# Optimization experiments

Measured on AMD Instinct MI355X. Metric: run time of the kernel, lower is better.

Reference implementation:

```python
import jax, jax.numpy as jnp
import numpy as np

C, H, W = 8, 8, 8
A = 6            # action_dim
LATENT = 64
HID = 64
GRU_IN = HID + A + LATENT  # 134


def _conv(x, w):
    return jax.lax.conv_general_dilated(
        x, w, (1, 1), 'VALID', dimension_numbers=('NCHW', 'OIHW', 'NCHW'))


def setup_inputs() -> dict:
    key = jax.random.key(0)
    ks = jax.random.split(key, 20)
    B, N, T = 64, 10, 128
    s_h = jax.random.normal(ks[0], (B, N, T, C, H, W), jnp.float32)
    a_h = jax.random.randint(ks[1], (B, N, T), 0, A).astype(jnp.int64)
    b_z = jax.random.normal(ks[2], (B, LATENT), jnp.float32)
    s = 0.05
    p = {
        'conv1_w': jax.random.normal(ks[3], (32, C, 3, 3)) * s,
        'conv1_b': jnp.zeros((32,)),
        'conv2_w': jax.random.normal(ks[4], (32, 32, 3, 3)) * s,
        'conv2_b': jnp.zeros((32,)),
        'fc_w': jax.random.normal(ks[5], (HID, 32 * 4 * 4)) * s,
        'fc_b': jnp.zeros((HID,)),
        'emb': jax.random.normal(ks[6], (A, A)) * s,
        'gru_wih': jax.random.normal(ks[7], (3 * HID, GRU_IN)) * s,
        'gru_whh': jax.random.normal(ks[8], (3 * HID, HID)) * s,
        'gru_bih': jnp.zeros((3 * HID,)),
        'gru_bhh': jnp.zeros((3 * HID,)),
        'mlp1_w': jax.random.normal(ks[9], (HID, HID)) * s,
        'mlp1_b': jnp.zeros((HID,)),
        'mlp2_w': jax.random.normal(ks[10], (A, HID)) * s,
        'mlp2_b': jnp.zeros((A,)),
    }
    return {'s_h': s_h, 'a_h': a_h, 'b_z': b_z, **p}


def reference(s_h, a_h, b_z, conv1_w, conv1_b, conv2_w, conv2_b, fc_w, fc_b,
              emb, gru_wih, gru_whh, gru_bih, gru_bhh,
              mlp1_w, mlp1_b, mlp2_w, mlp2_b):
    B, N = s_h.shape[0], s_h.shape[1]
    T = a_h.shape[2]
    BN = B * N

    # action mask, [B, N, T, 1]
    action_masks = (a_h != A - 1)[..., None].astype(jnp.float32)

    # --- state encoder on first frame only ---
    s0 = s_h[:, :, 0].reshape(BN, C, H, W)
    x = jax.nn.relu(_conv(s0, conv1_w) + conv1_b[:, None, None])
    x = jax.nn.relu(_conv(x, conv2_w) + conv2_b[:, None, None])
    x = x.reshape(BN, -1)                       # [BN, 512]
    state_emb = jax.nn.relu(x @ fc_w.T + fc_b)  # [BN, HID]

    bz = jnp.broadcast_to(b_z[:, None, :], (B, N, LATENT)).reshape(BN, LATENT)

    h0 = jnp.zeros((BN, HID), s_h.dtype)
    act0 = jnp.full((BN,), A - 1, jnp.int32)

    def step(carry, _):
        h, act = carry
        a_emb = emb[act]                                          # [BN, A]
        inp = jnp.concatenate([state_emb, a_emb, bz], axis=-1)    # [BN, GRU_IN]
        gx = inp @ gru_wih.T + gru_bih
        gh = h @ gru_whh.T + gru_bhh
        xr, xz, xn = jnp.split(gx, 3, axis=-1)
        hr, hz, hn = jnp.split(gh, 3, axis=-1)
        r = jax.nn.sigmoid(xr + hr)
        z = jax.nn.sigmoid(xz + hz)
        n = jnp.tanh(xn + r * hn)
        h_new = (1.0 - z) * n + z * h
        hid = jnp.tanh(h_new @ mlp1_w.T + mlp1_b)
        logits = hid @ mlp2_w.T + mlp2_b                          # [BN, A]
        next_act = jax.lax.stop_gradient(jnp.argmax(logits, axis=-1)).astype(jnp.int32)
        return (h_new, next_act), logits

    (_, _), logits_seq = jax.lax.scan(step, (h0, act0), None, length=T - 1)
    # logits_seq: [T-1, BN, A] -> [B, N, T-1, A]
    logits_all = jnp.transpose(logits_seq, (1, 0, 2)).reshape(B, N, T - 1, A)
    return logits_all, action_masks
```

## Files before the change

kernel.cpp:

```cpp
#include <hip/hip_runtime.h>

#define A_DIM 6
#define HID_D 64
#define LATENT_D 64
#define GRU_IN_D 134
#define T_STEPS 128
#define N_ENV 10
#define BN_TOT 640

typedef float f2 __attribute__((ext_vector_type(2)));

__device__ __forceinline__ float fast_sigmoid(float x) {
    return __builtin_amdgcn_rcpf(1.0f + __builtin_amdgcn_exp2f(-1.4426950408889634f * x));
}
__device__ __forceinline__ float fast_tanh(float x) {
    return 1.0f - 2.0f * __builtin_amdgcn_rcpf(1.0f + __builtin_amdgcn_exp2f(2.8853900817779268f * x));
}

template<int CTRL>
__device__ __forceinline__ float dppadd(float v) {
    int t = __builtin_amdgcn_update_dpp(0, __builtin_bit_cast(int, v), CTRL, 0xf, 0xf, true);
    return v + __builtin_bit_cast(float, t);
}
__device__ __forceinline__ float wave_reduce_add(float v) {
    v = dppadd<0x111>(v);
    v = dppadd<0x112>(v);
    v = dppadd<0x114>(v);
    v = dppadd<0x118>(v);
    v = dppadd<0x142>(v);
    v = dppadd<0x143>(v);
    return __builtin_bit_cast(float, __builtin_amdgcn_readlane(__builtin_bit_cast(int, v), 63));
}

__global__ __launch_bounds__(128, 1)
void policy_kernel(const float* __restrict__ s_h,
                   const int*   __restrict__ a_h,
                   const float* __restrict__ b_z,
                   const float* __restrict__ conv1_w, const float* __restrict__ conv1_b,
                   const float* __restrict__ conv2_w, const float* __restrict__ conv2_b,
                   const float* __restrict__ fc_w,    const float* __restrict__ fc_b,
                   const float* __restrict__ emb,
                   const float* __restrict__ gru_wih, const float* __restrict__ gru_whh,
                   const float* __restrict__ gru_bih, const float* __restrict__ gru_bhh,
                   const float* __restrict__ mlp1_w,  const float* __restrict__ mlp1_b,
                   const float* __restrict__ mlp2_w,  const float* __restrict__ mlp2_b,
                   float* __restrict__ logits_out, float* __restrict__ mask_out)
{
    __shared__ __align__(16) float s0[512];
    __shared__ __align__(16) float a1[1152];
    __shared__ __align__(16) float a2[512];
    __shared__ __align__(16) float pfc[128];
    __shared__ __align__(16) float semb[64];
    __shared__ __align__(16) float gxc[192];
    __shared__ __align__(16) float atab[6*192];
    __shared__ __align__(16) float hspec[6*64];

    const int bn  = blockIdx.x;
    const int tid = threadIdx.x;
    const int j   = tid & 63;
    const int w   = tid >> 6;

    mask_out[bn * T_STEPS + tid] = (a_h[bn * T_STEPS + tid] != (A_DIM - 1)) ? 1.0f : 0.0f;

    {
        const float* src = s_h + (size_t)bn * T_STEPS * 512;
        #pragma unroll
        for (int i = 0; i < 4; ++i) s0[tid + i * 128] = src[tid + i * 128];
    }
    __syncthreads();

    for (int i = tid; i < 1152; i += 128) {
        const int oc = i / 36, r = i % 36, oh = r / 6, ow = r % 6;
        float sum = conv1_b[oc];
        const float* wp = conv1_w + oc * 72;
        #pragma unroll
        for (int ic = 0; ic < 8; ++ic)
            #pragma unroll
            for (int kh = 0; kh < 3; ++kh)
                #pragma unroll
                for (int kw = 0; kw < 3; ++kw)
                    sum = fmaf(s0[ic * 64 + (oh + kh) * 8 + (ow + kw)],
                               wp[ic * 9 + kh * 3 + kw], sum);
        a1[i] = fmaxf(sum, 0.0f);
    }
    __syncthreads();

    for (int i = tid; i < 512; i += 128) {
        const int oc = i / 16, r = i % 16, oh = r / 4, ow = r % 4;
        float sum = conv2_b[oc];
        const float* wp = conv2_w + oc * 288;
        for (int ic = 0; ic < 32; ++ic)
            #pragma unroll
            for (int kh = 0; kh < 3; ++kh)
                #pragma unroll
                for (int kw = 0; kw < 3; ++kw)
                    sum = fmaf(a1[ic * 36 + (oh + kh) * 6 + (ow + kw)],
                               wp[ic * 9 + kh * 3 + kw], sum);
        a2[i] = fmaxf(sum, 0.0f);
    }
    __syncthreads();

    {
        const float* wp = fc_w + j * 512 + w * 256;
        const float* ap = a2 + w * 256;
        float s0a = 0.f, s1a = 0.f, s2a = 0.f, s3a = 0.f;
        for (int k = 0; k < 256; k += 4) {
            s0a = fmaf(ap[k + 0], wp[k + 0], s0a);
            s1a = fmaf(ap[k + 1], wp[k + 1], s1a);
            s2a = fmaf(ap[k + 2], wp[k + 2], s2a);
            s3a = fmaf(ap[k + 3], wp[k + 3], s3a);
        }
        pfc[tid] = (s0a + s1a) + (s2a + s3a);
    }
    __syncthreads();
    if (tid < 64) semb[tid] = fmaxf(pfc[tid] + pfc[tid + 64] + fc_b[tid], 0.0f);
    __syncthreads();

    {
        const float* bz = b_z + (size_t)(bn / N_ENV) * LATENT_D;
        for (int g = tid; g < 192; g += 128) {
            float sum = gru_bih[g] + ((g < 128) ? gru_bhh[g] : 0.0f);
            const float* wp = gru_wih + g * GRU_IN_D;
            for (int k = 0; k < 64; ++k) sum = fmaf(semb[k], wp[k], sum);
            for (int k = 0; k < 64; ++k) sum = fmaf(bz[k], wp[70 + k], sum);
            gxc[g] = sum;
        }
    }
    for (int i = tid; i < 6 * 192; i += 128) {
        const int a = i / 192, g = i % 192;
        float sum = 0.0f;
        #pragma unroll
        for (int q = 0; q < 6; ++q)
            sum = fmaf(emb[a * 6 + q], gru_wih[g * GRU_IN_D + 64 + q], sum);
        atab[i] = sum;
    }
    __syncthreads();

    if (w == 1) return;

    f2 wr[32], wz[32], wn[32], w1[32];
    {
        const float* pr = gru_whh + (size_t)j * 64;
        const float* pz = gru_whh + (size_t)(64 + j) * 64;
        const float* pn = gru_whh + (size_t)(128 + j) * 64;
        const float* p1 = mlp1_w + (size_t)j * 64;
        #pragma unroll
        for (int i = 0; i < 16; ++i) {
            float4 v;
            v = ((const float4*)pr)[i]; wr[2*i] = (f2){v.x, v.y}; wr[2*i+1] = (f2){v.z, v.w};
            v = ((const float4*)pz)[i]; wz[2*i] = (f2){v.x, v.y}; wz[2*i+1] = (f2){v.z, v.w};
            v = ((const float4*)pn)[i]; wn[2*i] = (f2){v.x, v.y}; wn[2*i+1] = (f2){v.z, v.w};
            v = ((const float4*)p1)[i]; w1[2*i] = (f2){v.x, v.y}; w1[2*i+1] = (f2){v.z, v.w};
        }
    }
    const float bhn = gru_bhh[128 + j];
    const float b1j = mlp1_b[j];
    float arx[6], azx[6], anx[6], m2c[6], b2[6];
    {
        const float gxr = gxc[j], gxz = gxc[64 + j], gxn = gxc[128 + j];
        #pragma unroll
        for (int a = 0; a < 6; ++a) {
            arx[a] = gxr + atab[a * 192 + j];
            azx[a] = gxz + atab[a * 192 + 64 + j];
            anx[a] = gxn + atab[a * 192 + 128 + j];
            m2c[a] = mlp2_w[a * 64 + j];
            b2[a] = mlp2_b[a];
        }
    }

    float ha[6];
    #pragma unroll
    for (int a = 0; a < 6; ++a) {
        const float r = fast_sigmoid(arx[a]);
        const float z = fast_sigmoid(azx[a]);
        const float n = fast_tanh(fmaf(r, bhn, anx[a]));
        ha[a] = fmaf(z, 0.0f - n, n);
    }
    __builtin_amdgcn_wave_barrier();
    #pragma unroll
    for (int a = 0; a < 6; ++a) hspec[a * 64 + j] = ha[a];
    __builtin_amdgcn_wave_barrier();

    int act = A_DIM - 1;
    float* lout = logits_out + (size_t)bn * (T_STEPS - 1) * A_DIM;

    for (int t = 0; t < T_STEPS - 1; ++t) {
        const float4* hb = (const float4*)(hspec + (act << 6));
        float hprev = ha[0];
        #pragma unroll
        for (int a = 1; a < 6; ++a) hprev = (act == a) ? ha[a] : hprev;

        f2 p1a = {0.f, 0.f}, p1b = {0.f, 0.f};
        f2 pr = {0.f, 0.f}, pz = {0.f, 0.f}, pn = {0.f, 0.f};
        #pragma unroll
        for (int i = 0; i < 16; ++i) {
            const float4 hv = hb[i];
            const f2 haa = (f2){hv.x, hv.y};
            const f2 hcc = (f2){hv.z, hv.w};
            p1a += haa * w1[2*i]; p1b += hcc * w1[2*i+1];
            pr += haa * wr[2*i]; pr += hcc * wr[2*i+1];
            pz += haa * wz[2*i]; pz += hcc * wz[2*i+1];
            pn += haa * wn[2*i]; pn += hcc * wn[2*i+1];
        }
        const f2 p1 = p1a + p1b;
        const float hid = fast_tanh(p1.x + p1.y + b1j);
        const float hr = pr.x + pr.y;
        const float hz = pz.x + pz.y;
        const float hn = pn.x + pn.y + bhn;

        const float l0 = wave_reduce_add(hid * m2c[0]) + b2[0];
        const float l1 = wave_reduce_add(hid * m2c[1]) + b2[1];
        const float l2 = wave_reduce_add(hid * m2c[2]) + b2[2];
        const float l3 = wave_reduce_add(hid * m2c[3]) + b2[3];
        const float l4 = wave_reduce_add(hid * m2c[4]) + b2[4];
        const float l5 = wave_reduce_add(hid * m2c[5]) + b2[5];

        #pragma unroll
        for (int a = 0; a < 6; ++a) {
            const float r = fast_sigmoid(arx[a] + hr);
            const float z = fast_sigmoid(azx[a] + hz);
            const float n = fast_tanh(fmaf(r, hn, anx[a]));
            ha[a] = fmaf(z, hprev - n, n);
        }
        __builtin_amdgcn_wave_barrier();
        #pragma unroll
        for (int a = 0; a < 6; ++a) hspec[a * 64 + j] = ha[a];
        __builtin_amdgcn_wave_barrier();

        float best = l0; int bi = 0;
        if (l1 > best) { best = l1; bi = 1; }
        if (l2 > best) { best = l2; bi = 2; }
        if (l3 > best) { best = l3; bi = 3; }
        if (l4 > best) { best = l4; bi = 4; }
        if (l5 > best) { best = l5; bi = 5; }
        act = bi;

        if (j < A_DIM) {
            const float outv = (j == 0) ? l0 : (j == 1) ? l1 : (j == 2) ? l2
                             : (j == 3) ? l3 : (j == 4) ? l4 : l5;
            lout[t * A_DIM + j] = outv;
        }
    }
}

extern "C" void kernel_launch(void* const* d_in, const int* in_sizes, int n_in,
                              void* d_out, int out_size, void* d_ws, size_t ws_size,
                              hipStream_t stream) {
    const float* s_h     = (const float*)d_in[0];
    const int*   a_h     = (const int*)  d_in[1];
    const float* b_z     = (const float*)d_in[2];
    const float* conv1_w = (const float*)d_in[3];
    const float* conv1_b = (const float*)d_in[4];
    const float* conv2_w = (const float*)d_in[5];
    const float* conv2_b = (const float*)d_in[6];
    const float* fc_w    = (const float*)d_in[7];
    const float* fc_b    = (const float*)d_in[8];
    const float* emb     = (const float*)d_in[9];
    const float* gru_wih = (const float*)d_in[10];
    const float* gru_whh = (const float*)d_in[11];
    const float* gru_bih = (const float*)d_in[12];
    const float* gru_bhh = (const float*)d_in[13];
    const float* mlp1_w  = (const float*)d_in[14];
    const float* mlp1_b  = (const float*)d_in[15];
    const float* mlp2_w  = (const float*)d_in[16];
    const float* mlp2_b  = (const float*)d_in[17];

    float* out = (float*)d_out;
    float* logits_out = out;
    float* mask_out   = out + (size_t)BN_TOT * (T_STEPS - 1) * A_DIM;

    policy_kernel<<<BN_TOT, 128, 0, stream>>>(
        s_h, a_h, b_z, conv1_w, conv1_b, conv2_w, conv2_b, fc_w, fc_b, emb,
        gru_wih, gru_whh, gru_bih, gru_bhh, mlp1_w, mlp1_b, mlp2_w, mlp2_b,
        logits_out, mask_out);
}
```

Measured before the change: 484.0 us.

## Shrink blocks to one wave and compute action-embedding projections in registers

Cuts each block from two waves to one 64-thread wave. The encoder prologue (conv1, conv2, fc) now runs serially on that single wave, and the split-K fc reduction through shared memory is gone. The shared atab table is replaced by per-lane register computation of the action-embedding contributions, which removes a shared buffer and a barrier. This frees CU resources that the idle second wave used to hold during the recurrent loop, at the cost of a longer prologue per block.

```diff
diff --git a/kernel.cpp b/kernel.cpp
--- a/kernel.cpp
+++ b/kernel.cpp
@@ -32,7 +32,7 @@
     return __builtin_bit_cast(float, __builtin_amdgcn_readlane(__builtin_bit_cast(int, v), 63));
 }
 
-__global__ __launch_bounds__(128, 1)
+__global__ __launch_bounds__(64) __attribute__((amdgpu_waves_per_eu(1, 1)))
 void policy_kernel(const float* __restrict__ s_h,
                    const int*   __restrict__ a_h,
                    const float* __restrict__ b_z,
@@ -49,27 +49,28 @@
     __shared__ __align__(16) float s0[512];
     __shared__ __align__(16) float a1[1152];
     __shared__ __align__(16) float a2[512];
-    __shared__ __align__(16) float pfc[128];
     __shared__ __align__(16) float semb[64];
     __shared__ __align__(16) float gxc[192];
-    __shared__ __align__(16) float atab[6*192];
     __shared__ __align__(16) float hspec[6*64];
 
     const int bn  = blockIdx.x;
     const int tid = threadIdx.x;
-    const int j   = tid & 63;
-    const int w   = tid >> 6;
-
-    mask_out[bn * T_STEPS + tid] = (a_h[bn * T_STEPS + tid] != (A_DIM - 1)) ? 1.0f : 0.0f;
+    const int j   = tid;
+
+    #pragma unroll
+    for (int i = 0; i < 2; ++i) {
+        const int t = tid + i * 64;
+        mask_out[bn * T_STEPS + t] = (a_h[bn * T_STEPS + t] != (A_DIM - 1)) ? 1.0f : 0.0f;
+    }
 
     {
         const float* src = s_h + (size_t)bn * T_STEPS * 512;
         #pragma unroll
-        for (int i = 0; i < 4; ++i) s0[tid + i * 128] = src[tid + i * 128];
-    }
-    __syncthreads();
-
-    for (int i = tid; i < 1152; i += 128) {
+        for (int i = 0; i < 8; ++i) s0[tid + i * 64] = src[tid + i * 64];
+    }
+    __syncthreads();
+
+    for (int i = tid; i < 1152; i += 64) {
         const int oc = i / 36, r = i % 36, oh = r / 6, ow = r % 6;
         float sum = conv1_b[oc];
         const float* wp = conv1_w + oc * 72;
@@ -85,7 +86,7 @@
     }
     __syncthreads();
 
-    for (int i = tid; i < 512; i += 128) {
+    for (int i = tid; i < 512; i += 64) {
         const int oc = i / 16, r = i % 16, oh = r / 4, ow = r % 4;
         float sum = conv2_b[oc];
         const float* wp = conv2_w + oc * 288;
@@ -101,24 +102,21 @@
     __syncthreads();
 
     {
-        const float* wp = fc_w + j * 512 + w * 256;
-        const float* ap = a2 + w * 256;
+        const float* wp = fc_w + j * 512;
         float s0a = 0.f, s1a = 0.f, s2a = 0.f, s3a = 0.f;
-        for (int k = 0; k < 256; k += 4) {
-            s0a = fmaf(ap[k + 0], wp[k + 0], s0a);
-            s1a = fmaf(ap[k + 1], wp[k + 1], s1a);
-            s2a = fmaf(ap[k + 2], wp[k + 2], s2a);
-            s3a = fmaf(ap[k + 3], wp[k + 3], s3a);
-        }
-        pfc[tid] = (s0a + s1a) + (s2a + s3a);
-    }
-    __syncthreads();
-    if (tid < 64) semb[tid] = fmaxf(pfc[tid] + pfc[tid + 64] + fc_b[tid], 0.0f);
+        for (int k = 0; k < 512; k += 4) {
+            s0a = fmaf(a2[k + 0], wp[k + 0], s0a);
+            s1a = fmaf(a2[k + 1], wp[k + 1], s1a);
+            s2a = fmaf(a2[k + 2], wp[k + 2], s2a);
+            s3a = fmaf(a2[k + 3], wp[k + 3], s3a);
+        }
+        semb[j] = fmaxf((s0a + s1a) + (s2a + s3a) + fc_b[j], 0.0f);
+    }
     __syncthreads();
 
     {
         const float* bz = b_z + (size_t)(bn / N_ENV) * LATENT_D;
-        for (int g = tid; g < 192; g += 128) {
+        for (int g = tid; g < 192; g += 64) {
             float sum = gru_bih[g] + ((g < 128) ? gru_bhh[g] : 0.0f);
             const float* wp = gru_wih + g * GRU_IN_D;
             for (int k = 0; k < 64; ++k) sum = fmaf(semb[k], wp[k], sum);
@@ -126,17 +124,7 @@
             gxc[g] = sum;
         }
     }
-    for (int i = tid; i < 6 * 192; i += 128) {
-        const int a = i / 192, g = i % 192;
-        float sum = 0.0f;
-        #pragma unroll
-        for (int q = 0; q < 6; ++q)
-            sum = fmaf(emb[a * 6 + q], gru_wih[g * GRU_IN_D + 64 + q], sum);
-        atab[i] = sum;
-    }
-    __syncthreads();
-
-    if (w == 1) return;
+    __syncthreads();
 
     f2 wr[32], wz[32], wn[32], w1[32];
     {
@@ -155,14 +143,30 @@
     }
     const float bhn = gru_bhh[128 + j];
     const float b1j = mlp1_b[j];
+
     float arx[6], azx[6], anx[6], m2c[6], b2[6];
     {
+        float wqr[6], wqz[6], wqn[6];
+        #pragma unroll
+        for (int q = 0; q < 6; ++q) {
+            wqr[q] = gru_wih[j * GRU_IN_D + 64 + q];
+            wqz[q] = gru_wih[(64 + j) * GRU_IN_D + 64 + q];
+            wqn[q] = gru_wih[(128 + j) * GRU_IN_D + 64 + q];
+        }
         const float gxr = gxc[j], gxz = gxc[64 + j], gxn = gxc[128 + j];
         #pragma unroll
         for (int a = 0; a < 6; ++a) {
-            arx[a] = gxr + atab[a * 192 + j];
-            azx[a] = gxz + atab[a * 192 + 64 + j];
-            anx[a] = gxn + atab[a * 192 + 128 + j];
+            float sr = 0.f, sz = 0.f, sn = 0.f;
+            #pragma unroll
+            for (int q = 0; q < 6; ++q) {
+                const float e = emb[a * 6 + q];
+                sr = fmaf(e, wqr[q], sr);
+                sz = fmaf(e, wqz[q], sz);
+                sn = fmaf(e, wqn[q], sn);
+            }
+            arx[a] = gxr + sr;
+            azx[a] = gxz + sz;
+            anx[a] = gxn + sn;
             m2c[a] = mlp2_w[a * 64 + j];
             b2[a] = mlp2_b[a];
         }
@@ -269,7 +273,7 @@
     float* logits_out = out;
     float* mask_out   = out + (size_t)BN_TOT * (T_STEPS - 1) * A_DIM;
 
-    policy_kernel<<<BN_TOT, 128, 0, stream>>>(
+    policy_kernel<<<BN_TOT, 64, 0, stream>>>(
         s_h, a_h, b_z, conv1_w, conv1_b, conv2_w, conv2_b, fc_w, fc_b, emb,
         gru_wih, gru_whh, gru_bih, gru_bhh, mlp1_w, mlp1_b, mlp2_w, mlp2_b,
         logits_out, mask_out);
```

Result: slower. 502.6 us (+3.8%).
